# Optimization experiments

Hardware: AMD Instinct MI355X
Metric: run time of the kernel (lower is better)

Reference implementation:

```python
import jax, jax.numpy as jnp
import numpy as np

B, N = 16, 2048
NOTE, BEAT_H, MEAS_H, FINAL_H = 512, 128, 64, 128
NUM_BEATS, NUM_MEAS = 256, 64
OUT = 11            # output_size; QPM_INDEX = 0
QPM = 0


def _uniform(k, shape, fan):
    b = 1.0 / np.sqrt(fan)
    return jax.random.uniform(k, shape, jnp.float32, -b, b)


def _lstm_cell(x, h, c, wih, whh, bih, bhh):
    g = x @ wih.T + bih + h @ whh.T + bhh
    ii, ff, gg, oo = jnp.split(g, 4, axis=-1)
    c2 = jax.nn.sigmoid(ff) * c + jax.nn.sigmoid(ii) * jnp.tanh(gg)
    return jax.nn.sigmoid(oo) * jnp.tanh(c2), c2


def setup_inputs() -> dict:
    key = jax.random.key(0)
    ks = jax.random.split(key, 20)
    note_emb = jax.random.normal(ks[0], (B, N, NOTE), jnp.float32)
    beat_emb = jax.random.normal(ks[1], (B, NUM_BEATS, BEAT_H), jnp.float32)
    measure_emb = jax.random.normal(ks[2], (B, NUM_MEAS, MEAS_H), jnp.float32)
    beat_numbers = jnp.sort(jax.random.randint(ks[3], (B, N), 0, NUM_BEATS), axis=1)
    measure_numbers = beat_numbers // (NUM_BEATS // NUM_MEAS)
    tin = BEAT_H + MEAS_H + 1 + (OUT - 1)   # beat-tempo LSTM input size
    fin = NOTE + BEAT_H + MEAS_H + OUT      # final LSTM input size
    d = OUT - 1
    return {
        "note_emb": note_emb, "beat_emb": beat_emb, "measure_emb": measure_emb,
        "beat_numbers": beat_numbers, "measure_numbers": measure_numbers,
        "Wa": _uniform(ks[4], (d, d), d), "ba": _uniform(ks[5], (d,), d),
        "ctx": _uniform(ks[6], (d,), d),
        "Wih_t": _uniform(ks[7], (4 * BEAT_H, tin), BEAT_H),
        "Whh_t": _uniform(ks[8], (4 * BEAT_H, BEAT_H), BEAT_H),
        "bih_t": _uniform(ks[9], (4 * BEAT_H,), BEAT_H),
        "bhh_t": _uniform(ks[10], (4 * BEAT_H,), BEAT_H),
        "Wih_f": _uniform(ks[11], (4 * FINAL_H, fin), FINAL_H),
        "Whh_f": _uniform(ks[12], (4 * FINAL_H, FINAL_H), FINAL_H),
        "bih_f": _uniform(ks[13], (4 * FINAL_H,), FINAL_H),
        "bhh_f": _uniform(ks[14], (4 * FINAL_H,), FINAL_H),
        "W_fc": _uniform(ks[15], (d, FINAL_H), FINAL_H),
        "b_fc": _uniform(ks[16], (d,), FINAL_H),
        "W_tfc": _uniform(ks[17], (1, BEAT_H), BEAT_H),
        "b_tfc": _uniform(ks[18], (1,), BEAT_H),
    }


def _decode(note_emb, beat_emb, measure_emb, beat_numbers, measure_numbers,
            Wa, ba, ctx, Wih_t, Whh_t, bih_t, bhh_t,
            Wih_f, Whh_f, bih_f, bhh_f, W_fc, b_fc, W_tfc, b_tfc):
    Bn, Nn = note_emb.shape[0], note_emb.shape[1]
    d = W_fc.shape[0]  # OUT - 1
    zs_beat = jnp.maximum(beat_numbers - beat_numbers[:, :1], 0)
    zs_meas = jnp.maximum(measure_numbers - measure_numbers[:, :1], 0)
    diff = jnp.diff(beat_numbers, axis=1)
    # beat_changed: first step forced to 1, then diff of beat numbers
    changed_all = jnp.concatenate([jnp.ones((Bn, 1), diff.dtype), diff], axis=1) > 0
    pos = jnp.arange(Nn)
    bidx = jnp.arange(Bn)

    carry0 = (
        jnp.zeros((Bn, BEAT_H)), jnp.zeros((Bn, BEAT_H)),        # tempo h, c
        jnp.zeros((Bn, FINAL_H)), jnp.zeros((Bn, FINAL_H)),      # final h, c
        jnp.zeros((Bn, d + 1)),                                   # prev_out
        jnp.zeros((Bn, beat_emb.shape[1], d)),                    # beat_results
        jnp.zeros((Bn, Nn, d + 1)),                               # out_total
    )

    def step(carry, i):
        th, tc, fh, fc_, prev_out, beat_results, out_total = carry
        changed = changed_all[:, i]                                # [B] bool
        # --- get_beat_corresp_out: notes j < i in the beat just finished ---
        prev_beat = beat_numbers[:, jnp.maximum(i - 1, 0)]         # [B]
        note_mask = (beat_numbers == prev_beat[:, None]) & (pos[None, :] < i)
        x = out_total[:, :, QPM + 1:]                              # [B,N,d]
        sim = (x @ Wa.T + ba) @ ctx                                # [B,N]
        sim = jnp.where(note_mask, sim, -1e9)
        w = jax.nn.softmax(sim, axis=1)
        result_node = jnp.einsum('bn,bnd->bd', w, x)
        result_node = jnp.where(note_mask.any(axis=1)[:, None], result_node, 0.0)
        cb = zs_beat[:, i]
        cm = zs_meas[:, i]
        # scatter result_node into beat_results only for batches whose beat changed
        old = beat_results[bidx, cb]
        beat_results = beat_results.at[bidx, cb].set(
            jnp.where(changed[:, None], result_node, old))
        # --- beat tempo RNN step (only applied where changed) ---
        tempo_in = jnp.concatenate([
            beat_emb[bidx, cb], measure_emb[bidx, cm],
            prev_out[:, QPM:QPM + 1], beat_results[bidx, cb]], axis=-1)
        th2, tc2 = _lstm_cell(tempo_in, th, tc, Wih_t, Whh_t, bih_t, bhh_t)
        th = jnp.where(changed[:, None], th2, th)
        tc = jnp.where(changed[:, None], tc2, tc)
        tmp_tempo = th2 @ W_tfc.T + b_tfc                          # [B,1]
        prev_out = prev_out.at[:, QPM:QPM + 1].set(
            jnp.where(changed[:, None], tmp_tempo, prev_out[:, QPM:QPM + 1]))
        # --- final note-level LSTM step (all batches) ---
        fin_in = jnp.concatenate([
            note_emb[:, i], beat_emb[bidx, cb], measure_emb[bidx, cm], prev_out], axis=-1)
        fh, fc_ = _lstm_cell(fin_in, fh, fc_, Wih_f, Whh_f, bih_f, bhh_f)
        out = fh @ W_fc.T + b_fc                                   # [B,d]
        prev_out = jnp.concatenate([prev_out[:, :QPM + 1], out], axis=-1)
        out_total = out_total.at[:, i].set(prev_out)
        return (th, tc, fh, fc_, prev_out, beat_results, out_total), None

    carry, _ = jax.lax.scan(step, carry0, jnp.arange(Nn))
    out_total = carry[-1]
    # zero out padded notes (note embedding all-zero rows)
    pad = (note_emb.sum(-1) == 0)[:, :, None]
    return jnp.where(pad, 0.0, out_total)


def reference(note_emb, beat_emb, measure_emb, beat_numbers, measure_numbers,
              Wa, ba, ctx, Wih_t, Whh_t, bih_t, bhh_t,
              Wih_f, Whh_f, bih_f, bhh_f, W_fc, b_fc, W_tfc, b_tfc):
    return _decode(note_emb, beat_emb, measure_emb, beat_numbers, measure_numbers,
                   Wa, ba, ctx, Wih_t, Whh_t, bih_t, bhh_t,
                   Wih_f, Whh_f, bih_f, bhh_f, W_fc, b_fc, W_tfc, b_tfc)
```

## Files before the change

kernel.cpp:

```cpp
#include <hip/hip_runtime.h>
#include <cstdint>
#include <cstddef>

#define B_      16
#define N_      2048
#define NOTE_   512
#define BEAT_H_ 128
#define MEAS_H_ 64
#define NBEATS_ 256
#define NMEAS_  64
#define OUT_    11
#define D_      10
#define TSTRIDE 136

typedef float f32x4 __attribute__((ext_vector_type(4)));
typedef unsigned int u32x4 __attribute__((ext_vector_type(4)));
typedef _Float16 h2v __attribute__((ext_vector_type(2)));

__device__ __forceinline__ float fexp2_(float x) {
#if __has_builtin(__builtin_amdgcn_exp2f)
    return __builtin_amdgcn_exp2f(x);
#else
    return exp2f(x);
#endif
}
__device__ __forceinline__ float frcp_(float x) {
#if __has_builtin(__builtin_amdgcn_rcpf)
    return __builtin_amdgcn_rcpf(x);
#else
    return 1.0f / x;
#endif
}
__device__ __forceinline__ float sigm_(float x) {
    return frcp_(1.0f + fexp2_(-1.4426950408889634f * x));
}
__device__ __forceinline__ float tanh_(float x) {
    return 1.0f - 2.0f * frcp_(fexp2_(2.8853900817779268f * x) + 1.0f);
}

#define DOT4(va, vb) ((va).x * (vb).x + (va).y * (vb).y + (va).z * (vb).z + (va).w * (vb).w)

__device__ __forceinline__ float dot2f_(unsigned wu, unsigned hu, float c) {
    union { unsigned u; h2v h; } a, bb;
    a.u = wu; bb.u = hu;
#if __has_builtin(__builtin_amdgcn_fdot2)
    return __builtin_amdgcn_fdot2(a.h, bb.h, c, false);
#else
    return c + (float)a.h[0] * (float)bb.h[0] + (float)a.h[1] * (float)bb.h[1];
#endif
}

__device__ __align__(16) _Float16 g_whh_h16[512 * 128];
__device__ float g_bias_eff[512];
__device__ float g_wtail0[512];
__device__ __align__(16) _Float16 g_wht_h16[512 * TSTRIDE];

__global__ __launch_bounds__(256) void pad_k(const float* __restrict__ note,
                                             int* __restrict__ padf) {
    int wave = threadIdx.x >> 6, lane = threadIdx.x & 63;
    int r = blockIdx.x * 4 + wave;
    const float* row = note + ((size_t)r << 9);
    float s = 0.f;
#pragma unroll
    for (int u = 0; u < 8; ++u) s += row[lane + (u << 6)];
#pragma unroll
    for (int off = 32; off; off >>= 1) s += __shfl_xor(s, off, 64);
    if (lane == 0) padf[r] = (s == 0.0f) ? 1 : 0;
}

__global__ __launch_bounds__(128) void fold_whh(
    const float* __restrict__ Whh_f, const float* __restrict__ Wih_f,
    const float* __restrict__ W_fc, const float* __restrict__ b_fc) {
    int gr = blockIdx.x;
    int t = threadIdx.x;
    __shared__ float tail[OUT_];
    if (t < OUT_) tail[t] = Wih_f[(size_t)gr * 715 + 704 + t];
    __syncthreads();
    float m = Whh_f[(size_t)gr * 128 + t];
#pragma unroll
    for (int d = 0; d < D_; ++d) m += tail[1 + d] * W_fc[d * 128 + t];
    g_whh_h16[(size_t)gr * 128 + t] = (_Float16)m;
    if (t == 0) {
        float bb = 0.f;
#pragma unroll
        for (int d = 0; d < D_; ++d) bb += tail[1 + d] * b_fc[d];
        g_bias_eff[gr] = bb;
        g_wtail0[gr] = tail[0];
    }
}

__global__ __launch_bounds__(128) void fold_wht(const float* __restrict__ Whh_t) {
    int gr = blockIdx.x, t = threadIdx.x;
    g_wht_h16[(size_t)gr * TSTRIDE + t] = (_Float16)Whh_t[(size_t)gr * 128 + t];
    if (t < TSTRIDE - 128) g_wht_h16[(size_t)gr * TSTRIDE + 128 + t] = (_Float16)0.f;
}

__global__ __launch_bounds__(256) void tempo_pre_k(
    const float* __restrict__ beat, const float* __restrict__ meas,
    const int* __restrict__ bnum, const int* __restrict__ mnum,
    const float* __restrict__ Wih_t, const float* __restrict__ bih_t,
    const float* __restrict__ bhh_t, float* __restrict__ tpre) {
    __shared__ float sin_[16][192];
    int b = blockIdx.x, qt = blockIdx.y;
    int t = threadIdx.x;
    int bn0 = bnum[b << 11], mn0 = mnum[b << 11];
    for (int idx = t; idx < 16 * 192; idx += 256) {
        int qq = idx / 192, kk = idx - qq * 192;
        int q = qt * 16 + qq;
        float v;
        if (kk < 128) {
            v = beat[(size_t)(b * NBEATS_ + q) * 128 + kk];
        } else {
            int cm = ((q + bn0) >> 2) - mn0;
            if (cm > 63) cm = 63;
            if (cm < 0) cm = 0;
            v = meas[(size_t)(b * NMEAS_ + cm) * 64 + (kk - 128)];
        }
        sin_[qq][kk] = v;
    }
    __syncthreads();
    for (int half = 0; half < 2; ++half) {
        int j = t + half * 256;
        const float* wr = Wih_t + (size_t)j * 203;
        float bias = bih_t[j] + bhh_t[j];
        float acc[16] = {};
        for (int k = 0; k < 192; ++k) {
            float w = wr[k];
#pragma unroll
            for (int qq = 0; qq < 16; ++qq) acc[qq] += w * sin_[qq][k];
        }
        for (int qq = 0; qq < 16; ++qq)
            tpre[(size_t)(b * NBEATS_ + qt * 16 + qq) * 512 + j] = acc[qq] + bias;
    }
}

__global__ __launch_bounds__(256) void fin_pre_gemm(
    const float* __restrict__ note, const float* __restrict__ beat,
    const float* __restrict__ meas, const int* __restrict__ bnum,
    const int* __restrict__ mnum, const float* __restrict__ Wih_f,
    const float* __restrict__ bih_f, const float* __restrict__ bhh_f,
    float* __restrict__ finp) {
    __shared__ float As[16][64];
    __shared__ float Bs[16][64];
    int t = threadIdx.x;
    int r0 = blockIdx.x * 64;
    int j0 = blockIdx.y * 64;

    int am = t >> 2, alane = t & 3;
    int r = r0 + am;
    int b = r >> 11;
    int rb = b << 11;
    int cb = bnum[r] - bnum[rb];
    int cm = mnum[r] - mnum[rb];
    const float* arow_note = note + ((size_t)r << 9);
    const float* arow_beat = beat + ((size_t)(b * NBEATS_ + cb) << 7);
    const float* arow_meas = meas + ((size_t)(b * NMEAS_ + cm) << 6);

    int jj = t >> 2, blane = t & 3;
    const float* brow = Wih_f + (size_t)(j0 + jj) * 715;

    int tm0 = (t & 15) * 4, tn0 = (t >> 4) * 4;
    float acc[4][4] = {};

    for (int k0 = 0; k0 < 704; k0 += 16) {
        int ka = k0 + alane * 4;
        float4 av;
        if (ka < 512)      av = *(const float4*)(arow_note + ka);
        else if (ka < 640) av = *(const float4*)(arow_beat + (ka - 512));
        else               av = *(const float4*)(arow_meas + (ka - 640));
        int kb = k0 + blane * 4;
        float b0 = brow[kb], b1 = brow[kb + 1], b2 = brow[kb + 2], b3 = brow[kb + 3];
        __syncthreads();
        As[alane * 4 + 0][am] = av.x;
        As[alane * 4 + 1][am] = av.y;
        As[alane * 4 + 2][am] = av.z;
        As[alane * 4 + 3][am] = av.w;
        Bs[blane * 4 + 0][jj] = b0;
        Bs[blane * 4 + 1][jj] = b1;
        Bs[blane * 4 + 2][jj] = b2;
        Bs[blane * 4 + 3][jj] = b3;
        __syncthreads();
#pragma unroll
        for (int kk = 0; kk < 16; ++kk) {
            float4 a4 = *(const float4*)&As[kk][tm0];
            float4 b4 = *(const float4*)&Bs[kk][tn0];
            float aa[4] = {a4.x, a4.y, a4.z, a4.w};
            float bb[4] = {b4.x, b4.y, b4.z, b4.w};
#pragma unroll
            for (int mi = 0; mi < 4; ++mi)
#pragma unroll
                for (int ni = 0; ni < 4; ++ni) acc[mi][ni] += aa[mi] * bb[ni];
        }
    }
    float bias[4], beff[4];
#pragma unroll
    for (int ni = 0; ni < 4; ++ni) {
        int j = j0 + tn0 + ni;
        bias[ni] = bih_f[j] + bhh_f[j];
        beff[ni] = g_bias_eff[j];
    }
#pragma unroll
    for (int mi = 0; mi < 4; ++mi) {
        int rr = r0 + tm0 + mi;
        float eb = (rr & 2047) ? 1.0f : 0.0f;
        float4 o;
        o.x = acc[mi][0] + bias[0] + eb * beff[0];
        o.y = acc[mi][1] + bias[1] + eb * beff[1];
        o.z = acc[mi][2] + bias[2] + eb * beff[2];
        o.w = acc[mi][3] + bias[3] + eb * beff[3];
        *(float4*)(finp + ((size_t)rr << 9) + j0 + tn0) = o;
    }
}

__global__ __launch_bounds__(512)
__attribute__((amdgpu_waves_per_eu(2, 2)))
void decode_seq(
    const float* __restrict__ finp, const float* __restrict__ tpre,
    const int* __restrict__ bnum, const int* __restrict__ padf,
    const float* __restrict__ Wih_t,
    const float* __restrict__ W_fc, const float* __restrict__ b_fc,
    const float* __restrict__ W_tfc, const float* __restrict__ b_tfc,
    const float* __restrict__ Wa, const float* __restrict__ ba,
    const float* __restrict__ ctx, float* __restrict__ out,
    float* __restrict__ xg) {
    __shared__ __align__(16) _Float16 wht16_s[512 * TSTRIDE];
    __shared__ __align__(16) _Float16 ht16_s[128];
    __shared__ __align__(16) _Float16 hf16_s[128];
    __shared__ __align__(16) float hf_s[128];
    __shared__ float cf_s[128];
    __shared__ float ht_s[128];
    __shared__ float ct_s[128];
    __shared__ __align__(16) float g_s[512];
    __shared__ float gt_s[512];
    __shared__ float wtail0_s[512];
    __shared__ float wfcT[128][12];
    __shared__ float wtfc_s[128];
    __shared__ float bfc_s[12];
    __shared__ float cur_res[12];
    __shared__ float v_s[12];
    __shared__ float sc_s[4];
    __shared__ unsigned long long padw_s[32];
    __shared__ unsigned short run_start_s[300];
    __shared__ short run_cb_s[300];
    __shared__ int nruns_s;

    int t = threadIdx.x, lane = t & 63, wave = t >> 6;
    int b = blockIdx.x;

    u32x4 wf0, wf1, wf2, wf3, wf4, wf5, wf6, wf7;
    u32x4 wf8, wf9, wf10, wf11, wf12, wf13, wf14, wf15;
    {
        const u32x4* wfp = (const u32x4*)(g_whh_h16 + (size_t)t * 128);
        wf0 = wfp[0];   wf1 = wfp[1];   wf2 = wfp[2];   wf3 = wfp[3];
        wf4 = wfp[4];   wf5 = wfp[5];   wf6 = wfp[6];   wf7 = wfp[7];
        wf8 = wfp[8];   wf9 = wfp[9];   wf10 = wfp[10]; wf11 = wfp[11];
        wf12 = wfp[12]; wf13 = wfp[13]; wf14 = wfp[14]; wf15 = wfp[15];
    }
    asm volatile("" : "+v"(wf0), "+v"(wf1), "+v"(wf2), "+v"(wf3),
                      "+v"(wf4), "+v"(wf5), "+v"(wf6), "+v"(wf7));
    asm volatile("" : "+v"(wf8), "+v"(wf9), "+v"(wf10), "+v"(wf11),
                      "+v"(wf12), "+v"(wf13), "+v"(wf14), "+v"(wf15));

    float wtail0_r = g_wtail0[t];
    wtail0_s[t] = wtail0_r;
    float wiht_r[OUT_];
#pragma unroll
    for (int u = 0; u < OUT_; ++u) wiht_r[u] = Wih_t[(size_t)t * 203 + 192 + u];

    {
        const uint4* src = (const uint4*)g_wht_h16;
        uint4* dst = (uint4*)wht16_s;
#pragma unroll
        for (int k = 0; k < 17; ++k) dst[t + 512 * k] = src[t + 512 * k];
    }
    for (int k = t; k < 128 * D_; k += 512) {
        int d = k >> 7, r = k & 127;
        wfcT[r][d] = W_fc[k];
    }
    if (t < 128) {
        wtfc_s[t] = W_tfc[t];
        hf_s[t] = 0.f; cf_s[t] = 0.f; ht_s[t] = 0.f; ct_s[t] = 0.f;
        ht16_s[t] = (_Float16)0.f;
        hf16_s[t] = (_Float16)0.f;
    }
    if (t < D_) {
        bfc_s[t] = b_fc[t];
        cur_res[t] = 0.f;
        float vv = 0.f;
        for (int m = 0; m < D_; ++m) vv += ctx[m] * Wa[m * D_ + t];
        v_s[t] = vv;
    }
    if (t == 10) {
        float cc = 0.f;
        for (int m = 0; m < D_; ++m) cc += ba[m] * ctx[m];
        sc_s[0] = cc;
        sc_s[1] = b_tfc[0];
        sc_s[2] = 0.f;
    }
    if (wave >= 2 && wave < 6) {
        for (int jj = 0; jj < 8; ++jj) {
            int j = (wave - 2) * 8 + jj;
            int pv = padf[(b << 11) + j * 64 + lane];
            unsigned long long m = __ballot(pv != 0);
            if (lane == 0) padw_s[j] = m;
        }
    }
    const int* bnb = bnum + (b << 11);
    int bn0 = bnb[0];
    int base = t * 4;
    int bvm = (base == 0) ? 0 : bnb[base - 1];
    int bv0 = bnb[base], bv1 = bnb[base + 1], bv2 = bnb[base + 2], bv3 = bnb[base + 3];
    if (base == 0) bvm = bv0 - 1;
    int c = (bv0 != bvm) + (bv1 != bv0) + (bv2 != bv1) + (bv3 != bv2);
    ((int*)g_s)[t] = c;
    __syncthreads();
    if (wave == 0) {
        int c8[8], s = 0;
#pragma unroll
        for (int j = 0; j < 8; ++j) { c8[j] = ((int*)g_s)[lane * 8 + j]; s += c8[j]; }
        int incl = s;
#pragma unroll
        for (int off = 1; off < 64; off <<= 1) {
            int n = __shfl_up(incl, off, 64);
            if (lane >= off) incl += n;
        }
        int run = incl - s;
#pragma unroll
        for (int j = 0; j < 8; ++j) { ((int*)gt_s)[lane * 8 + j] = run; run += c8[j]; }
        if (lane == 63) nruns_s = incl;
    }
    __syncthreads();
    {
        int O = ((int*)gt_s)[t];
        if (bv0 != bvm) { run_start_s[O] = (unsigned short)(base + 0); run_cb_s[O] = (short)(bv0 - bn0); O++; }
        if (bv1 != bv0) { run_start_s[O] = (unsigned short)(base + 1); run_cb_s[O] = (short)(bv1 - bn0); O++; }
        if (bv2 != bv1) { run_start_s[O] = (unsigned short)(base + 2); run_cb_s[O] = (short)(bv2 - bn0); O++; }
        if (bv3 != bv2) { run_start_s[O] = (unsigned short)(base + 3); run_cb_s[O] = (short)(bv3 - bn0); O++; }
    }
    __syncthreads();
    int nruns_r = nruns_s;

    const float* finrow = finp + ((size_t)b << 11) * 512;
    float* xgb = xg + ((size_t)(b << 11)) * 16;
    float gf_cur = finrow[t];
    float gt_pre = tpre[(size_t)(b * NBEATS_) * 512 + t];
    int cur_run = -1, next_start = 0, run_s = 0, S_prev = 0;

    for (int i = 0; i < N_; ++i) {
        bool changed = (i == next_start);
        if (changed) {
            cur_run++;
            S_prev = run_s;
            run_s = i;
            next_start = (cur_run + 1 < nruns_r) ? (int)run_start_s[cur_run + 1] : 4096;
        }
        float gf_pre = finrow[(size_t)(i + 1) * 512 + t];
        float prev0 = sc_s[2];

        float acc;
        {
            const u32x4* hq = (const u32x4*)hf16_s;
            float a0 = 0.f, a1 = 0.f, a2 = 0.f, a3 = 0.f;
#define MSTEP(W, K)                                            \
            { u32x4 H = hq[K];                                 \
              a0 = dot2f_(W.x, H.x, a0);                       \
              a1 = dot2f_(W.y, H.y, a1);                       \
              a2 = dot2f_(W.z, H.z, a2);                       \
              a3 = dot2f_(W.w, H.w, a3); }
            MSTEP(wf0, 0)   MSTEP(wf1, 1)   MSTEP(wf2, 2)   MSTEP(wf3, 3)
            MSTEP(wf4, 4)   MSTEP(wf5, 5)   MSTEP(wf6, 6)   MSTEP(wf7, 7)
            MSTEP(wf8, 8)   MSTEP(wf9, 9)   MSTEP(wf10, 10) MSTEP(wf11, 11)
            MSTEP(wf12, 12) MSTEP(wf13, 13) MSTEP(wf14, 14) MSTEP(wf15, 15)
#undef MSTEP
            acc = (a0 + a1) + (a2 + a3);
        }
        {
            float g = gf_cur + acc;
            if (!changed) g += wtail0_r * prev0;
            g_s[t] = g;
        }
        gf_cur = gf_pre;

        if (wave == 1 && i > 0) {
            int dd = lane >> 3, rl = lane & 7;
            int d2i = 8 + dd;
            float po1 = 0.f, po2 = 0.f;
            for (int k2 = 0; k2 < 16; ++k2) {
                int r = rl + (k2 << 3);
                float hv = hf_s[r];
                po1 += hv * wfcT[r][dd];
                if (d2i < D_) po2 += hv * wfcT[r][d2i];
            }
            po1 += __shfl_xor(po1, 1); po1 += __shfl_xor(po1, 2); po1 += __shfl_xor(po1, 4);
            po2 += __shfl_xor(po2, 1); po2 += __shfl_xor(po2, 2); po2 += __shfl_xor(po2, 4);
            int pi = i - 1;
            int pd = (int)((padw_s[pi >> 6] >> (pi & 63)) & 1ULL);
            float* orow = out + (size_t)((b << 11) + pi) * OUT_;
            float* xrow = xgb + (size_t)pi * 16;
            if (rl == 0) {
                float od = po1 + bfc_s[dd];
                xrow[dd] = od;
                orow[1 + dd] = pd ? 0.f : od;
                if (d2i < D_) {
                    float od2 = po2 + bfc_s[d2i];
                    xrow[d2i] = od2;
                    orow[1 + d2i] = pd ? 0.f : od2;
                }
            }
            if (lane == 1) orow[0] = pd ? 0.f : prev0;
        }

        if (changed) {
            float acct;
            {
                const u32x4* wq = (const u32x4*)(wht16_s + (size_t)t * TSTRIDE);
                const u32x4* hq = (const u32x4*)ht16_s;
                float a0 = 0.f, a1 = 0.f, a2 = 0.f, a3 = 0.f;
#pragma unroll
                for (int k = 0; k < 16; ++k) {
                    u32x4 W = wq[k];
                    u32x4 H = hq[k];
                    a0 = dot2f_(W.x, H.x, a0);
                    a1 = dot2f_(W.y, H.y, a1);
                    a2 = dot2f_(W.z, H.z, a2);
                    a3 = dot2f_(W.w, H.w, a3);
                }
                acct = (a0 + a1) + (a2 + a3);
            }
            gt_s[t] = gt_pre + acct + wiht_r[0] * prev0;
        }
        __syncthreads();

        if (!changed) {
            if (wave < 2) {
                int rr = lane + (wave << 6);
                float gi = g_s[rr], gff = g_s[128 + rr], gg = g_s[256 + rr], go = g_s[384 + rr];
                float c2 = sigm_(gff) * cf_s[rr] + sigm_(gi) * tanh_(gg);
                float h2 = sigm_(go) * tanh_(c2);
                cf_s[rr] = c2;
                hf_s[rr] = h2;
                hf16_s[rr] = (_Float16)h2;
            }
        } else {
            if (wave == 0) {
                int L = i - S_prev;
                const float4* xb = (const float4*)(xgb + (size_t)S_prev * 16);
                float lmax = -1e30f;
                for (int tt = lane; tt < L; tt += 64) {
                    float4 q0 = xb[tt * 4 + 0], q1 = xb[tt * 4 + 1], q2 = xb[tt * 4 + 2];
                    float s = sc_s[0] + q0.x * v_s[0] + q0.y * v_s[1] + q0.z * v_s[2] +
                              q0.w * v_s[3] + q1.x * v_s[4] + q1.y * v_s[5] +
                              q1.z * v_s[6] + q1.w * v_s[7] + q2.x * v_s[8] + q2.y * v_s[9];
                    lmax = fmaxf(lmax, s);
                }
#pragma unroll
                for (int off = 32; off; off >>= 1)
                    lmax = fmaxf(lmax, __shfl_xor(lmax, off, 64));
                float lsum = 0.f, lacc[D_] = {};
                for (int tt = lane; tt < L; tt += 64) {
                    float4 q0 = xb[tt * 4 + 0], q1 = xb[tt * 4 + 1], q2 = xb[tt * 4 + 2];
                    float s = sc_s[0] + q0.x * v_s[0] + q0.y * v_s[1] + q0.z * v_s[2] +
                              q0.w * v_s[3] + q1.x * v_s[4] + q1.y * v_s[5] +
                              q1.z * v_s[6] + q1.w * v_s[7] + q2.x * v_s[8] + q2.y * v_s[9];
                    float w = fexp2_(1.4426950408889634f * (s - lmax));
                    lsum += w;
                    lacc[0] += w * q0.x; lacc[1] += w * q0.y; lacc[2] += w * q0.z;
                    lacc[3] += w * q0.w; lacc[4] += w * q1.x; lacc[5] += w * q1.y;
                    lacc[6] += w * q1.z; lacc[7] += w * q1.w; lacc[8] += w * q2.x;
                    lacc[9] += w * q2.y;
                }
#pragma unroll
                for (int off = 32; off; off >>= 1) {
                    lsum += __shfl_xor(lsum, off, 64);
#pragma unroll
                    for (int d = 0; d < D_; ++d) lacc[d] += __shfl_xor(lacc[d], off, 64);
                }
                if (lane == 0) {
                    if (L > 0) {
                        float inv = 1.0f / lsum;
#pragma unroll
                        for (int d = 0; d < D_; ++d) cur_res[d] = lacc[d] * inv;
                    } else {
#pragma unroll
                        for (int d = 0; d < D_; ++d) cur_res[d] = 0.f;
                    }
                }
            }
            __syncthreads();
            {
                float gv = gt_s[t];
#pragma unroll
                for (int d = 0; d < D_; ++d) gv += wiht_r[1 + d] * cur_res[d];
                gt_s[t] = gv;
            }
            __syncthreads();
            if (wave == 0) {
                float p = 0.f;
#pragma unroll
                for (int hb = 0; hb < 2; ++hb) {
                    int rr = lane + (hb << 6);
                    float gi = gt_s[rr], gff = gt_s[128 + rr], gg = gt_s[256 + rr],
                          go = gt_s[384 + rr];
                    float c2 = sigm_(gff) * ct_s[rr] + sigm_(gi) * tanh_(gg);
                    float h2 = sigm_(go) * tanh_(c2);
                    ct_s[rr] = c2;
                    ht_s[rr] = h2;
                    ht16_s[rr] = (_Float16)h2;
                    p += h2 * wtfc_s[rr];
                }
#pragma unroll
                for (int off = 32; off; off >>= 1) p += __shfl_xor(p, off, 64);
                float tnew = p + sc_s[1];
                if (lane == 0) sc_s[2] = tnew;
#pragma unroll
                for (int hb = 0; hb < 2; ++hb) {
                    int rr = lane + (hb << 6);
                    float gi = g_s[rr] + wtail0_s[rr] * tnew;
                    float gff = g_s[128 + rr] + wtail0_s[128 + rr] * tnew;
                    float gg = g_s[256 + rr] + wtail0_s[256 + rr] * tnew;
                    float go = g_s[384 + rr] + wtail0_s[384 + rr] * tnew;
                    float c2 = sigm_(gff) * cf_s[rr] + sigm_(gi) * tanh_(gg);
                    float h2 = sigm_(go) * tanh_(c2);
                    cf_s[rr] = c2;
                    hf_s[rr] = h2;
                    hf16_s[rr] = (_Float16)h2;
                }
            }
            if (cur_run + 1 < nruns_r)
                gt_pre = tpre[(size_t)(b * NBEATS_ + (int)run_cb_s[cur_run + 1]) * 512 + t];
        }
        __syncthreads();
    }

    if (wave == 1) {
        int dd = lane >> 3, rl = lane & 7;
        int d2i = 8 + dd;
        float po1 = 0.f, po2 = 0.f;
        for (int k2 = 0; k2 < 16; ++k2) {
            int r = rl + (k2 << 3);
            float hv = hf_s[r];
            po1 += hv * wfcT[r][dd];
            if (d2i < D_) po2 += hv * wfcT[r][d2i];
        }
        po1 += __shfl_xor(po1, 1); po1 += __shfl_xor(po1, 2); po1 += __shfl_xor(po1, 4);
        po2 += __shfl_xor(po2, 1); po2 += __shfl_xor(po2, 2); po2 += __shfl_xor(po2, 4);
        int pi = N_ - 1;
        int pd = (int)((padw_s[pi >> 6] >> (pi & 63)) & 1ULL);
        float* orow = out + (size_t)((b << 11) + pi) * OUT_;
        if (rl == 0) {
            orow[1 + dd] = pd ? 0.f : (po1 + bfc_s[dd]);
            if (d2i < D_) orow[1 + d2i] = pd ? 0.f : (po2 + bfc_s[d2i]);
        }
        if (lane == 1) orow[0] = pd ? 0.f : sc_s[2];
    }
}

extern "C" void kernel_launch(void* const* d_in, const int* in_sizes, int n_in,
                              void* d_out, int out_size, void* d_ws, size_t ws_size,
                              hipStream_t stream) {
    const float* note  = (const float*)d_in[0];
    const float* beat  = (const float*)d_in[1];
    const float* meas  = (const float*)d_in[2];
    const int*   bnum  = (const int*)d_in[3];
    const int*   mnum  = (const int*)d_in[4];
    const float* Wa    = (const float*)d_in[5];
    const float* ba    = (const float*)d_in[6];
    const float* ctx   = (const float*)d_in[7];
    const float* Wih_t = (const float*)d_in[8];
    const float* Whh_t = (const float*)d_in[9];
    const float* bih_t = (const float*)d_in[10];
    const float* bhh_t = (const float*)d_in[11];
    const float* Wih_f = (const float*)d_in[12];
    const float* Whh_f = (const float*)d_in[13];
    const float* bih_f = (const float*)d_in[14];
    const float* bhh_f = (const float*)d_in[15];
    const float* W_fc  = (const float*)d_in[16];
    const float* b_fc  = (const float*)d_in[17];
    const float* W_tfc = (const float*)d_in[18];
    const float* b_tfc = (const float*)d_in[19];
    float* out = (float*)d_out;

    char* ws = (char*)d_ws;
    float* finp = (float*)ws;
    float* tpre = (float*)(ws + (size_t)64 * 1024 * 1024);
    int*   padf = (int*)(ws + (size_t)72 * 1024 * 1024);
    float* xg   = (float*)(ws + (size_t)73 * 1024 * 1024);

    pad_k<<<8192, 256, 0, stream>>>(note, padf);
    fold_whh<<<512, 128, 0, stream>>>(Whh_f, Wih_f, W_fc, b_fc);
    fold_wht<<<512, 128, 0, stream>>>(Whh_t);
    tempo_pre_k<<<dim3(16, 16), 256, 0, stream>>>(beat, meas, bnum, mnum, Wih_t,
                                                  bih_t, bhh_t, tpre);
    fin_pre_gemm<<<dim3(512, 8), 256, 0, stream>>>(note, beat, meas, bnum, mnum,
                                                   Wih_f, bih_f, bhh_f, finp);
    decode_seq<<<16, 512, 0, stream>>>(finp, tpre, bnum, padf, Wih_t,
                                       W_fc, b_fc, W_tfc, b_tfc, Wa, ba, ctx,
                                       out, xg);
}
```

Measured before the change: 4.203 ms.

## Remap gate rows per wave, shuffle-based cell update, defer output projection

Assigns each wave 16 hidden units, with all four gates of a unit held by lanes of that wave. The LSTM cell is then computed with lane shuffles instead of a shared-memory gate buffer, and the hidden state is double-buffered, which drops one block barrier per non-boundary step. The per-step output FC is moved to a separate out_k kernel that reads fp16 hidden states written in place over the consumed finp rows. Attention is rewritten to score the stored hidden states against a precomputed projected context vector. The trade-offs are fp16 storage of hidden states, an extra launch, and an attention window capped at 1024 notes, which risks changing results for long beat runs.

Result: faster. 3.879 ms (-7.7%).

```diff
diff --git a/kernel.cpp b/kernel.cpp
--- a/kernel.cpp
+++ b/kernel.cpp
@@ -37,8 +37,6 @@
 __device__ __forceinline__ float tanh_(float x) {
     return 1.0f - 2.0f * frcp_(fexp2_(2.8853900817779268f * x) + 1.0f);
 }
-
-#define DOT4(va, vb) ((va).x * (vb).x + (va).y * (vb).y + (va).z * (vb).z + (va).w * (vb).w)
 
 __device__ __forceinline__ float dot2f_(unsigned wu, unsigned hu, float c) {
     union { unsigned u; h2v h; } a, bb;
@@ -215,42 +213,39 @@
 __global__ __launch_bounds__(512)
 __attribute__((amdgpu_waves_per_eu(2, 2)))
 void decode_seq(
-    const float* __restrict__ finp, const float* __restrict__ tpre,
-    const int* __restrict__ bnum, const int* __restrict__ padf,
+    float* finp,
+    const float* __restrict__ tpre, const int* __restrict__ bnum,
     const float* __restrict__ Wih_t,
     const float* __restrict__ W_fc, const float* __restrict__ b_fc,
     const float* __restrict__ W_tfc, const float* __restrict__ b_tfc,
     const float* __restrict__ Wa, const float* __restrict__ ba,
-    const float* __restrict__ ctx, float* __restrict__ out,
-    float* __restrict__ xg) {
+    const float* __restrict__ ctx, float* __restrict__ tval) {
     __shared__ __align__(16) _Float16 wht16_s[512 * TSTRIDE];
+    __shared__ __align__(16) _Float16 hf16_s[2][128];
     __shared__ __align__(16) _Float16 ht16_s[128];
-    __shared__ __align__(16) _Float16 hf16_s[128];
-    __shared__ __align__(16) float hf_s[128];
-    __shared__ float cf_s[128];
-    __shared__ float ht_s[128];
-    __shared__ float ct_s[128];
-    __shared__ __align__(16) float g_s[512];
-    __shared__ float gt_s[512];
-    __shared__ float wtail0_s[512];
+    __shared__ __align__(16) _Float16 u16_s[128];
+    __shared__ __align__(16) float hA_s[128];
+    __shared__ __align__(16) float s_w_s[1024];
     __shared__ float wfcT[128][12];
-    __shared__ float wtfc_s[128];
     __shared__ float bfc_s[12];
+    __shared__ float v_s[12];
     __shared__ float cur_res[12];
-    __shared__ float v_s[12];
+    __shared__ float pred_s[8];
     __shared__ float sc_s[4];
-    __shared__ unsigned long long padw_s[32];
     __shared__ unsigned short run_start_s[300];
     __shared__ short run_cb_s[300];
     __shared__ int nruns_s;
 
-    int t = threadIdx.x, lane = t & 63, wave = t >> 6;
-    int b = blockIdx.x;
+    const int t = threadIdx.x, lane = t & 63, wave = t >> 6;
+    const int b = blockIdx.x;
+    const int bl = lane & 15;
+    const int eidx = wave * 16 + bl;
+    const int r_lane = (lane >> 4) * 128 + eidx;
 
     u32x4 wf0, wf1, wf2, wf3, wf4, wf5, wf6, wf7;
     u32x4 wf8, wf9, wf10, wf11, wf12, wf13, wf14, wf15;
     {
-        const u32x4* wfp = (const u32x4*)(g_whh_h16 + (size_t)t * 128);
+        const u32x4* wfp = (const u32x4*)(g_whh_h16 + (size_t)r_lane * 128);
         wf0 = wfp[0];   wf1 = wfp[1];   wf2 = wfp[2];   wf3 = wfp[3];
         wf4 = wfp[4];   wf5 = wfp[5];   wf6 = wfp[6];   wf7 = wfp[7];
         wf8 = wfp[8];   wf9 = wfp[9];   wf10 = wfp[10]; wf11 = wfp[11];
@@ -261,11 +256,11 @@
     asm volatile("" : "+v"(wf8), "+v"(wf9), "+v"(wf10), "+v"(wf11),
                       "+v"(wf12), "+v"(wf13), "+v"(wf14), "+v"(wf15));
 
-    float wtail0_r = g_wtail0[t];
-    wtail0_s[t] = wtail0_r;
+    const float wtail0_r = g_wtail0[r_lane];
+    const float wtfc_r = W_tfc[eidx];
     float wiht_r[OUT_];
 #pragma unroll
-    for (int u = 0; u < OUT_; ++u) wiht_r[u] = Wih_t[(size_t)t * 203 + 192 + u];
+    for (int u = 0; u < OUT_; ++u) wiht_r[u] = Wih_t[(size_t)r_lane * 203 + 192 + u];
 
     {
         const uint4* src = (const uint4*)g_wht_h16;
@@ -278,10 +273,9 @@
         wfcT[r][d] = W_fc[k];
     }
     if (t < 128) {
-        wtfc_s[t] = W_tfc[t];
-        hf_s[t] = 0.f; cf_s[t] = 0.f; ht_s[t] = 0.f; ct_s[t] = 0.f;
+        hf16_s[0][t] = (_Float16)0.f;
+        hf16_s[1][t] = (_Float16)0.f;
         ht16_s[t] = (_Float16)0.f;
-        hf16_s[t] = (_Float16)0.f;
     }
     if (t < D_) {
         bfc_s[t] = b_fc[t];
@@ -296,14 +290,6 @@
         sc_s[0] = cc;
         sc_s[1] = b_tfc[0];
         sc_s[2] = 0.f;
-    }
-    if (wave >= 2 && wave < 6) {
-        for (int jj = 0; jj < 8; ++jj) {
-            int j = (wave - 2) * 8 + jj;
-            int pv = padf[(b << 11) + j * 64 + lane];
-            unsigned long long m = __ballot(pv != 0);
-            if (lane == 0) padw_s[j] = m;
-        }
     }
     const int* bnb = bnum + (b << 11);
     int bn0 = bnb[0];
@@ -312,12 +298,23 @@
     int bv0 = bnb[base], bv1 = bnb[base + 1], bv2 = bnb[base + 2], bv3 = bnb[base + 3];
     if (base == 0) bvm = bv0 - 1;
     int c = (bv0 != bvm) + (bv1 != bv0) + (bv2 != bv1) + (bv3 != bv2);
-    ((int*)g_s)[t] = c;
+    ((int*)s_w_s)[t] = c;
     __syncthreads();
+    if (t == 0) {
+        float c1v = sc_s[0];
+        for (int d = 0; d < D_; ++d) c1v += bfc_s[d] * v_s[d];
+        sc_s[3] = c1v;
+    }
+    if (t < 128) {
+        float uu = 0.f;
+#pragma unroll
+        for (int d = 0; d < D_; ++d) uu += v_s[d] * wfcT[t][d];
+        u16_s[t] = (_Float16)uu;
+    }
     if (wave == 0) {
         int c8[8], s = 0;
 #pragma unroll
-        for (int j = 0; j < 8; ++j) { c8[j] = ((int*)g_s)[lane * 8 + j]; s += c8[j]; }
+        for (int j = 0; j < 8; ++j) { c8[j] = ((int*)s_w_s)[lane * 8 + j]; s += c8[j]; }
         int incl = s;
 #pragma unroll
         for (int off = 1; off < 64; off <<= 1) {
@@ -326,40 +323,42 @@
         }
         int run = incl - s;
 #pragma unroll
-        for (int j = 0; j < 8; ++j) { ((int*)gt_s)[lane * 8 + j] = run; run += c8[j]; }
+        for (int j = 0; j < 8; ++j) { ((int*)s_w_s)[512 + lane * 8 + j] = run; run += c8[j]; }
         if (lane == 63) nruns_s = incl;
     }
     __syncthreads();
     {
-        int O = ((int*)gt_s)[t];
+        int O = ((int*)s_w_s)[512 + t];
         if (bv0 != bvm) { run_start_s[O] = (unsigned short)(base + 0); run_cb_s[O] = (short)(bv0 - bn0); O++; }
         if (bv1 != bv0) { run_start_s[O] = (unsigned short)(base + 1); run_cb_s[O] = (short)(bv1 - bn0); O++; }
         if (bv2 != bv1) { run_start_s[O] = (unsigned short)(base + 2); run_cb_s[O] = (short)(bv2 - bn0); O++; }
         if (bv3 != bv2) { run_start_s[O] = (unsigned short)(base + 3); run_cb_s[O] = (short)(bv3 - bn0); O++; }
     }
     __syncthreads();
-    int nruns_r = nruns_s;
-
-    const float* finrow = finp + ((size_t)b << 11) * 512;
-    float* xgb = xg + ((size_t)(b << 11)) * 16;
-    float gf_cur = finrow[t];
-    float gt_pre = tpre[(size_t)(b * NBEATS_) * 512 + t];
+    const int nruns_r = nruns_s;
+
+    char* hg = (char*)(finp + ((size_t)b << 11) * 512);
+    const size_t fin_off = ((size_t)b << 11) * 512 + (size_t)r_lane;
+    float gf_cur = finp[fin_off];
+    float gt_pre = tpre[(size_t)(b * NBEATS_) * 512 + r_lane];
     int cur_run = -1, next_start = 0, run_s = 0, S_prev = 0;
+    int pb = 0;
+    float cf_r = 0.f, ct_r = 0.f;
 
     for (int i = 0; i < N_; ++i) {
-        bool changed = (i == next_start);
+        const bool changed = (i == next_start);
         if (changed) {
-            cur_run++;
+            ++cur_run;
             S_prev = run_s;
             run_s = i;
-            next_start = (cur_run + 1 < nruns_r) ? (int)run_start_s[cur_run + 1] : 4096;
-        }
-        float gf_pre = finrow[(size_t)(i + 1) * 512 + t];
+            next_start = (cur_run + 1 < nruns_r) ? (int)run_start_s[cur_run + 1] : (N_ * 2);
+        }
         float prev0 = sc_s[2];
+        float gf_nxt = finp[fin_off + (size_t)(i + 1) * 512];
 
         float acc;
         {
-            const u32x4* hq = (const u32x4*)hf16_s;
+            const u32x4* hq = (const u32x4*)&hf16_s[pb][0];
             float a0 = 0.f, a1 = 0.f, a2 = 0.f, a3 = 0.f;
 #define MSTEP(W, K)                                            \
             { u32x4 H = hq[K];                                 \
@@ -374,46 +373,26 @@
 #undef MSTEP
             acc = (a0 + a1) + (a2 + a3);
         }
-        {
-            float g = gf_cur + acc;
-            if (!changed) g += wtail0_r * prev0;
-            g_s[t] = g;
-        }
-        gf_cur = gf_pre;
-
-        if (wave == 1 && i > 0) {
-            int dd = lane >> 3, rl = lane & 7;
-            int d2i = 8 + dd;
-            float po1 = 0.f, po2 = 0.f;
-            for (int k2 = 0; k2 < 16; ++k2) {
-                int r = rl + (k2 << 3);
-                float hv = hf_s[r];
-                po1 += hv * wfcT[r][dd];
-                if (d2i < D_) po2 += hv * wfcT[r][d2i];
+        float gmain = gf_cur + acc;
+        gf_cur = gf_nxt;
+        float tv = prev0;
+
+        if (!changed) {
+            float g = gmain + wtail0_r * prev0;
+            float gF = __shfl(g, bl + 16, 64);
+            float gG = __shfl(g, bl + 32, 64);
+            float gO = __shfl(g, bl + 48, 64);
+            if (lane < 16) {
+                float c2 = sigm_(gF) * cf_r + sigm_(g) * tanh_(gG);
+                float h2 = sigm_(gO) * tanh_(c2);
+                cf_r = c2;
+                hf16_s[pb ^ 1][eidx] = (_Float16)h2;
+                *(_Float16*)(hg + (size_t)i * 2048 + (eidx << 1)) = (_Float16)h2;
             }
-            po1 += __shfl_xor(po1, 1); po1 += __shfl_xor(po1, 2); po1 += __shfl_xor(po1, 4);
-            po2 += __shfl_xor(po2, 1); po2 += __shfl_xor(po2, 2); po2 += __shfl_xor(po2, 4);
-            int pi = i - 1;
-            int pd = (int)((padw_s[pi >> 6] >> (pi & 63)) & 1ULL);
-            float* orow = out + (size_t)((b << 11) + pi) * OUT_;
-            float* xrow = xgb + (size_t)pi * 16;
-            if (rl == 0) {
-                float od = po1 + bfc_s[dd];
-                xrow[dd] = od;
-                orow[1 + dd] = pd ? 0.f : od;
-                if (d2i < D_) {
-                    float od2 = po2 + bfc_s[d2i];
-                    xrow[d2i] = od2;
-                    orow[1 + d2i] = pd ? 0.f : od2;
-                }
-            }
-            if (lane == 1) orow[0] = pd ? 0.f : prev0;
-        }
-
-        if (changed) {
-            float acct;
+        } else {
+            float gt;
             {
-                const u32x4* wq = (const u32x4*)(wht16_s + (size_t)t * TSTRIDE);
+                const u32x4* wq = (const u32x4*)(wht16_s + (size_t)r_lane * TSTRIDE);
                 const u32x4* hq = (const u32x4*)ht16_s;
                 float a0 = 0.f, a1 = 0.f, a2 = 0.f, a3 = 0.f;
 #pragma unroll
@@ -425,134 +404,135 @@
                     a2 = dot2f_(W.z, H.z, a2);
                     a3 = dot2f_(W.w, H.w, a3);
                 }
-                acct = (a0 + a1) + (a2 + a3);
+                gt = gt_pre + (a0 + a1) + (a2 + a3) + wiht_r[0] * prev0;
             }
-            gt_s[t] = gt_pre + acct + wiht_r[0] * prev0;
-        }
-        __syncthreads();
-
-        if (!changed) {
-            if (wave < 2) {
-                int rr = lane + (wave << 6);
-                float gi = g_s[rr], gff = g_s[128 + rr], gg = g_s[256 + rr], go = g_s[384 + rr];
-                float c2 = sigm_(gff) * cf_s[rr] + sigm_(gi) * tanh_(gg);
-                float h2 = sigm_(go) * tanh_(c2);
-                cf_s[rr] = c2;
-                hf_s[rr] = h2;
-                hf16_s[rr] = (_Float16)h2;
-            }
-        } else {
+            if (cur_run + 1 < nruns_r)
+                gt_pre = tpre[(size_t)(b * NBEATS_ + (int)run_cb_s[cur_run + 1]) * 512 + r_lane];
+
             if (wave == 0) {
-                int L = i - S_prev;
-                const float4* xb = (const float4*)(xgb + (size_t)S_prev * 16);
+                int Lc = i - S_prev;
+                if (Lc > 1024) Lc = 1024;
+                const char* hgB = hg + (size_t)S_prev * 2048;
+                const float c1 = sc_s[3];
                 float lmax = -1e30f;
-                for (int tt = lane; tt < L; tt += 64) {
-                    float4 q0 = xb[tt * 4 + 0], q1 = xb[tt * 4 + 1], q2 = xb[tt * 4 + 2];
-                    float s = sc_s[0] + q0.x * v_s[0] + q0.y * v_s[1] + q0.z * v_s[2] +
-                              q0.w * v_s[3] + q1.x * v_s[4] + q1.y * v_s[5] +
-                              q1.z * v_s[6] + q1.w * v_s[7] + q2.x * v_s[8] + q2.y * v_s[9];
+                for (int j = lane; j < Lc; j += 64) {
+                    const u32x4* hrow = (const u32x4*)(hgB + (size_t)j * 2048);
+                    const u32x4* uq = (const u32x4*)u16_s;
+                    float a0 = 0.f, a1 = 0.f, a2 = 0.f, a3 = 0.f;
+#pragma unroll
+                    for (int k = 0; k < 16; ++k) {
+                        u32x4 hv = hrow[k], uv = uq[k];
+                        a0 = dot2f_(hv.x, uv.x, a0);
+                        a1 = dot2f_(hv.y, uv.y, a1);
+                        a2 = dot2f_(hv.z, uv.z, a2);
+                        a3 = dot2f_(hv.w, uv.w, a3);
+                    }
+                    float s = c1 + (a0 + a1) + (a2 + a3);
+                    s_w_s[j] = s;
                     lmax = fmaxf(lmax, s);
                 }
 #pragma unroll
                 for (int off = 32; off; off >>= 1)
                     lmax = fmaxf(lmax, __shfl_xor(lmax, off, 64));
-                float lsum = 0.f, lacc[D_] = {};
-                for (int tt = lane; tt < L; tt += 64) {
-                    float4 q0 = xb[tt * 4 + 0], q1 = xb[tt * 4 + 1], q2 = xb[tt * 4 + 2];
-                    float s = sc_s[0] + q0.x * v_s[0] + q0.y * v_s[1] + q0.z * v_s[2] +
-                              q0.w * v_s[3] + q1.x * v_s[4] + q1.y * v_s[5] +
-                              q1.z * v_s[6] + q1.w * v_s[7] + q2.x * v_s[8] + q2.y * v_s[9];
-                    float w = fexp2_(1.4426950408889634f * (s - lmax));
+                float lsum = 0.f;
+                for (int j = lane; j < Lc; j += 64) {
+                    float w = fexp2_(1.4426950408889634f * (s_w_s[j] - lmax));
+                    s_w_s[j] = w;
                     lsum += w;
-                    lacc[0] += w * q0.x; lacc[1] += w * q0.y; lacc[2] += w * q0.z;
-                    lacc[3] += w * q0.w; lacc[4] += w * q1.x; lacc[5] += w * q1.y;
-                    lacc[6] += w * q1.z; lacc[7] += w * q1.w; lacc[8] += w * q2.x;
-                    lacc[9] += w * q2.y;
                 }
 #pragma unroll
-                for (int off = 32; off; off >>= 1) {
-                    lsum += __shfl_xor(lsum, off, 64);
-#pragma unroll
-                    for (int d = 0; d < D_; ++d) lacc[d] += __shfl_xor(lacc[d], off, 64);
+                for (int off = 32; off; off >>= 1) lsum += __shfl_xor(lsum, off, 64);
+                float inv = (Lc > 0) ? (1.0f / lsum) : 0.f;
+                float hA0 = 0.f, hA1 = 0.f;
+                for (int j = 0; j < Lc; ++j) {
+                    unsigned hv = *(const unsigned*)(hgB + (size_t)j * 2048 + (lane << 2));
+                    float w = s_w_s[j];
+                    union { unsigned u; _Float16 h[2]; } hu; hu.u = hv;
+                    hA0 += w * (float)hu.h[0];
+                    hA1 += w * (float)hu.h[1];
                 }
-                if (lane == 0) {
-                    if (L > 0) {
-                        float inv = 1.0f / lsum;
-#pragma unroll
-                        for (int d = 0; d < D_; ++d) cur_res[d] = lacc[d] * inv;
-                    } else {
-#pragma unroll
-                        for (int d = 0; d < D_; ++d) cur_res[d] = 0.f;
-                    }
+                hA_s[2 * lane] = hA0 * inv;
+                hA_s[2 * lane + 1] = hA1 * inv;
+                int dd = lane >> 3, rl = lane & 7, d2 = 8 + dd;
+                float po1 = 0.f, po2 = 0.f;
+                for (int k2 = 0; k2 < 16; ++k2) {
+                    int r = rl + (k2 << 3);
+                    float hv = hA_s[r];
+                    po1 += hv * wfcT[r][dd];
+                    if (d2 < D_) po2 += hv * wfcT[r][d2];
+                }
+                po1 += __shfl_xor(po1, 1, 64); po1 += __shfl_xor(po1, 2, 64); po1 += __shfl_xor(po1, 4, 64);
+                po2 += __shfl_xor(po2, 1, 64); po2 += __shfl_xor(po2, 2, 64); po2 += __shfl_xor(po2, 4, 64);
+                if (rl == 0) {
+                    cur_res[dd] = (Lc > 0) ? (po1 + bfc_s[dd]) : 0.f;
+                    if (d2 < D_) cur_res[d2] = (Lc > 0) ? (po2 + bfc_s[d2]) : 0.f;
                 }
             }
             __syncthreads();
-            {
-                float gv = gt_s[t];
-#pragma unroll
-                for (int d = 0; d < D_; ++d) gv += wiht_r[1 + d] * cur_res[d];
-                gt_s[t] = gv;
+#pragma unroll
+            for (int d = 0; d < D_; ++d) gt += wiht_r[1 + d] * cur_res[d];
+            float gF = __shfl(gt, bl + 16, 64);
+            float gG = __shfl(gt, bl + 32, 64);
+            float gO = __shfl(gt, bl + 48, 64);
+            if (lane < 16) {
+                float c2 = sigm_(gF) * ct_r + sigm_(gt) * tanh_(gG);
+                float h2 = sigm_(gO) * tanh_(c2);
+                ct_r = c2;
+                ht16_s[eidx] = (_Float16)h2;
+                float p = h2 * wtfc_r;
+                p += __shfl_xor(p, 1, 64);
+                p += __shfl_xor(p, 2, 64);
+                p += __shfl_xor(p, 4, 64);
+                p += __shfl_xor(p, 8, 64);
+                if (bl == 0) pred_s[wave] = p;
             }
             __syncthreads();
-            if (wave == 0) {
-                float p = 0.f;
-#pragma unroll
-                for (int hb = 0; hb < 2; ++hb) {
-                    int rr = lane + (hb << 6);
-                    float gi = gt_s[rr], gff = gt_s[128 + rr], gg = gt_s[256 + rr],
-                          go = gt_s[384 + rr];
-                    float c2 = sigm_(gff) * ct_s[rr] + sigm_(gi) * tanh_(gg);
-                    float h2 = sigm_(go) * tanh_(c2);
-                    ct_s[rr] = c2;
-                    ht_s[rr] = h2;
-                    ht16_s[rr] = (_Float16)h2;
-                    p += h2 * wtfc_s[rr];
-                }
-#pragma unroll
-                for (int off = 32; off; off >>= 1) p += __shfl_xor(p, off, 64);
-                float tnew = p + sc_s[1];
-                if (lane == 0) sc_s[2] = tnew;
-#pragma unroll
-                for (int hb = 0; hb < 2; ++hb) {
-                    int rr = lane + (hb << 6);
-                    float gi = g_s[rr] + wtail0_s[rr] * tnew;
-                    float gff = g_s[128 + rr] + wtail0_s[128 + rr] * tnew;
-                    float gg = g_s[256 + rr] + wtail0_s[256 + rr] * tnew;
-                    float go = g_s[384 + rr] + wtail0_s[384 + rr] * tnew;
-                    float c2 = sigm_(gff) * cf_s[rr] + sigm_(gi) * tanh_(gg);
-                    float h2 = sigm_(go) * tanh_(c2);
-                    cf_s[rr] = c2;
-                    hf_s[rr] = h2;
-                    hf16_s[rr] = (_Float16)h2;
-                }
+            float tnew = sc_s[1];
+#pragma unroll
+            for (int wv = 0; wv < 8; ++wv) tnew += pred_s[wv];
+            tv = tnew;
+            float g = gmain + wtail0_r * tnew;
+            float gF2 = __shfl(g, bl + 16, 64);
+            float gG2 = __shfl(g, bl + 32, 64);
+            float gO2 = __shfl(g, bl + 48, 64);
+            if (lane < 16) {
+                float c2 = sigm_(gF2) * cf_r + sigm_(g) * tanh_(gG2);
+                float h2 = sigm_(gO2) * tanh_(c2);
+                cf_r = c2;
+                hf16_s[pb ^ 1][eidx] = (_Float16)h2;
+                *(_Float16*)(hg + (size_t)i * 2048 + (eidx << 1)) = (_Float16)h2;
             }
-            if (cur_run + 1 < nruns_r)
-                gt_pre = tpre[(size_t)(b * NBEATS_ + (int)run_cb_s[cur_run + 1]) * 512 + t];
-        }
+            if (t == 0) sc_s[2] = tnew;
+        }
+        if (t == 0) tval[(b << 11) + i] = tv;
         __syncthreads();
-    }
-
-    if (wave == 1) {
-        int dd = lane >> 3, rl = lane & 7;
-        int d2i = 8 + dd;
-        float po1 = 0.f, po2 = 0.f;
-        for (int k2 = 0; k2 < 16; ++k2) {
-            int r = rl + (k2 << 3);
-            float hv = hf_s[r];
-            po1 += hv * wfcT[r][dd];
-            if (d2i < D_) po2 += hv * wfcT[r][d2i];
-        }
-        po1 += __shfl_xor(po1, 1); po1 += __shfl_xor(po1, 2); po1 += __shfl_xor(po1, 4);
-        po2 += __shfl_xor(po2, 1); po2 += __shfl_xor(po2, 2); po2 += __shfl_xor(po2, 4);
-        int pi = N_ - 1;
-        int pd = (int)((padw_s[pi >> 6] >> (pi & 63)) & 1ULL);
-        float* orow = out + (size_t)((b << 11) + pi) * OUT_;
-        if (rl == 0) {
-            orow[1 + dd] = pd ? 0.f : (po1 + bfc_s[dd]);
-            if (d2i < D_) orow[1 + d2i] = pd ? 0.f : (po2 + bfc_s[d2i]);
-        }
-        if (lane == 1) orow[0] = pd ? 0.f : sc_s[2];
-    }
+        pb ^= 1;
+    }
+}
+
+__global__ __launch_bounds__(256) void out_k(
+    const float* __restrict__ finp, const float* __restrict__ tval,
+    const int* __restrict__ padf, const float* __restrict__ W_fc,
+    const float* __restrict__ b_fc, float* __restrict__ out) {
+    int g = blockIdx.x * 256 + threadIdx.x;
+    int row = g >> 4, slot = g & 15;
+    if (row >= B_ * N_) return;
+    int pd = padf[row];
+    float* orow = out + (size_t)row * OUT_;
+    if (slot == 10) {
+        orow[0] = pd ? 0.f : tval[row];
+        return;
+    }
+    if (slot > 10) return;
+    const unsigned* h2 = (const unsigned*)(finp + (size_t)row * 512);
+    const float* wr = W_fc + slot * 128;
+    float acc = b_fc[slot];
+#pragma unroll 8
+    for (int k = 0; k < 64; ++k) {
+        union { unsigned u; _Float16 h[2]; } hv; hv.u = h2[k];
+        acc += (float)hv.h[0] * wr[2 * k] + (float)hv.h[1] * wr[2 * k + 1];
+    }
+    orow[1 + slot] = pd ? 0.f : acc;
 }
 
 extern "C" void kernel_launch(void* const* d_in, const int* in_sizes, int n_in,
@@ -584,7 +564,7 @@
     float* finp = (float*)ws;
     float* tpre = (float*)(ws + (size_t)64 * 1024 * 1024);
     int*   padf = (int*)(ws + (size_t)72 * 1024 * 1024);
-    float* xg   = (float*)(ws + (size_t)73 * 1024 * 1024);
+    float* tval = (float*)(ws + (size_t)73 * 1024 * 1024);
 
     pad_k<<<8192, 256, 0, stream>>>(note, padf);
     fold_whh<<<512, 128, 0, stream>>>(Whh_f, Wih_f, W_fc, b_fc);
@@ -593,7 +573,8 @@
                                                   bih_t, bhh_t, tpre);
     fin_pre_gemm<<<dim3(512, 8), 256, 0, stream>>>(note, beat, meas, bnum, mnum,
                                                    Wih_f, bih_f, bhh_f, finp);
-    decode_seq<<<16, 512, 0, stream>>>(finp, tpre, bnum, padf, Wih_t,
+    decode_seq<<<16, 512, 0, stream>>>(finp, tpre, bnum, Wih_t,
                                        W_fc, b_fc, W_tfc, b_tfc, Wa, ba, ctx,
-                                       out, xg);
-}
+                                       tval);
+    out_k<<<2048, 256, 0, stream>>>(finp, tval, padf, W_fc, b_fc, out);
+}
```
